# Optimization experiments

Hardware: AMD Instinct MI355X
Metric: run time of the kernel (lower is better)

The kernel has to match this reference:

```python
import jax, jax.numpy as jnp
import numpy as np

THETA_LO = 0.001
THETA_HI = 2.0
N_SUBSTEPS = 1
B, K, U, P, H, L = 256, 512, 16, 64, 256, 64
TH = 2 * P  # theta_dim: [decay rates | drives]


def setup_inputs() -> dict:
    key = jax.random.key(0)
    ks = jax.random.split(key, 12)
    s = 0.05
    return {
        "y0": jax.random.uniform(ks[0], (B, P), jnp.float32),
        "u_seq": jax.random.normal(ks[1], (B, K, U), jnp.float32),
        "dt_seq": jax.random.uniform(ks[2], (B, K), jnp.float32, 0.01, 0.1),
        "W_lift": jax.random.normal(ks[3], (L, U + P), jnp.float32) * s,
        "b_lift": jnp.zeros((L,), jnp.float32),
        "W_ih": jax.random.normal(ks[4], (3 * H, L), jnp.float32) * s,
        "b_ih": jnp.zeros((3 * H,), jnp.float32),
        "W_hh": jax.random.normal(ks[5], (3 * H, H), jnp.float32) * s,
        "b_hh": jnp.zeros((3 * H,), jnp.float32),
        "W_head": jax.random.normal(ks[6], (TH, H), jnp.float32) * s,
        "b_head": jnp.zeros((TH,), jnp.float32),
        "jump": jax.random.normal(ks[7], (U, P), jnp.float32) * s,
    }


def reference(y0, u_seq, dt_seq, W_lift, b_lift, W_ih, b_ih, W_hh, b_hh,
              W_head, b_head, jump):
    Pd = y0.shape[-1]

    def rhs(y, theta):
        # linear production/decay scaffold: y' = drive - decay * y
        return theta[:, Pd:] - theta[:, :Pd] * y

    def gru_cell(x, h):
        gi = x @ W_ih.T + b_ih            # [B, 3H]
        gh = h @ W_hh.T + b_hh            # [B, 3H]
        ir, iz, inn = jnp.split(gi, 3, axis=-1)
        hr, hz, hn = jnp.split(gh, 3, axis=-1)
        r = jax.nn.sigmoid(ir + hr)
        z = jax.nn.sigmoid(iz + hz)
        n = jnp.tanh(inn + r * hn)
        return (1.0 - z) * n + z * h

    def step(carry, inp):
        y_prev, h = carry
        u_k, dt_k = inp                   # [B,U], [B]
        y_in = jax.lax.stop_gradient(y_prev)  # .detach() in original
        feat = jnp.concatenate([u_k, y_in], axis=-1)
        x = jax.nn.silu(feat @ W_lift.T + b_lift)
        h = gru_cell(x, h)
        raw = h @ W_head.T + b_head
        theta = THETA_LO + (THETA_HI - THETA_LO) * jax.nn.sigmoid(raw)
        y = y_prev + u_k @ jump           # jump update
        hdt = (dt_k / N_SUBSTEPS)[:, None]
        for _ in range(N_SUBSTEPS):       # RK4 substeps
            k1 = rhs(y, theta)
            k2 = rhs(y + 0.5 * hdt * k1, theta)
            k3 = rhs(y + 0.5 * hdt * k2, theta)
            k4 = rhs(y + hdt * k3, theta)
            y = y + hdt / 6.0 * (k1 + 2.0 * k2 + 2.0 * k3 + k4)
        y = jnp.maximum(y, 0.0)           # clamp_min(0)
        return (y, h), (y, theta)

    Bd = y0.shape[0]
    Hd = W_hh.shape[1]
    h0 = jnp.zeros((Bd, Hd), y0.dtype)
    u_t = jnp.swapaxes(u_seq, 0, 1)       # [K,B,U]
    dt_t = dt_seq.T                       # [K,B]
    _, (y_out, th_out) = jax.lax.scan(step, (y0, h0), (u_t, dt_t))
    return jnp.swapaxes(y_out, 0, 1), jnp.swapaxes(th_out, 0, 1)
```

## Files before the change

kernel.cpp:

```cpp
#include <hip/hip_runtime.h>
#include <hip/hip_bf16.h>

#define BB 256
#define KK 512
#define UU 16
#define PP 64
#define HH 256
#define LL 64
#define THD 128
#define MB 16
#define NS 8
#define NG 16
#define NBLK (NG*NS)
#define NT 256

#define WHH_F 0
#define WIH_F 48
#define WHD_F 60
#define WLF_F 124
#define NFRG 136

#define FP2 104
#define XP2 72
#define TP2 132

#define HX_BUF 65536
#define HX_GRP 4096

typedef _Float16 f16;
typedef _Float16 f16x8 __attribute__((ext_vector_type(8)));
typedef float f32x4 __attribute__((ext_vector_type(4)));
typedef unsigned u32x4 __attribute__((ext_vector_type(4)));

__device__ __forceinline__ float sigm(float x) { return 1.f / (1.f + __expf(-x)); }
__device__ __forceinline__ f32x4 MFMA(f16x8 a, f16x8 b, f32x4 c) {
  return __builtin_amdgcn_mfma_f32_16x16x32_f16(a, b, c, 0, 0, 0);
}

#define GLD16_S(dst, p) \
  asm volatile("global_load_dwordx4 %0, %1, off sc0 sc1" : "=&v"(dst) : "v"(p))
#define GSTH_S(p, v) \
  asm volatile("global_store_short %0, %1, off sc0 sc1" :: "v"(p), "v"(v) : "memory")
#define VM0() do { asm volatile("s_waitcnt vmcnt(0)" ::: "memory"); \
                   __builtin_amdgcn_sched_barrier(0); } while (0)

struct SM {
  alignas(16) f16 frg[NFRG * 512];
  alignas(16) f16 x_M[MB * XP2];
  alignas(16) f16 f_M[MB * FP2];
  alignas(16) float th[MB * TP2];
  alignas(16) float ubuf[2][MB][UU];
  alignas(16) float jmp[UU * PP];
  float dts[2][MB];
  float bihs[96], bhhs[96];
  float bhead[THD];
  float blift[LL];
};

__device__ __forceinline__ void put_frag(f16* frg, int base_f, int ntK, int nt,
                                         int n16, int k, float v) {
  int kk = k >> 5, lgp = (k >> 3) & 3, j = k & 7;
  int lane = lgp * 16 + n16;
  frg[(base_f + nt * ntK + kk) * 512 + lane * 8 + j] = (f16)v;
}

#define FRG(FID) (*(const f16x8*)&sm.frg[(FID) * 512 + lane * 8])

__global__ __launch_bounds__(NT) void odernn_coop(
    const float* __restrict__ y0, const float* __restrict__ u_seq,
    const float* __restrict__ dt_seq, const float* __restrict__ W_lift,
    const float* __restrict__ b_lift, const float* __restrict__ W_ih,
    const float* __restrict__ b_ih, const float* __restrict__ W_hh,
    const float* __restrict__ b_hh, const float* __restrict__ W_head,
    const float* __restrict__ b_head, const float* __restrict__ jump,
    f16* __restrict__ hx,
    float* __restrict__ out_y, float* __restrict__ out_th) {
  __shared__ SM sm;
  const int t = threadIdx.x;
  const int lane = t & 63, wv = t >> 6, lm = lane & 15, lg = lane >> 4;
  const int bid = blockIdx.x, g = bid >> 3, ns = bid & 7;
  const int g16 = g * MB;
  const int ub = 32 * ns;

  for (int e = t; e < 96 * 256; e += NT) {
    int l = e >> 8, k = e & 255;
    int gate = l >> 5, ul = l & 31;
    put_frag(sm.frg, WHH_F, 8, l >> 4, l & 15, k, W_hh[(gate * 256 + ub + ul) * 256 + k]);
  }
  for (int e = t; e < 96 * 64; e += NT) {
    int l = e >> 6, k = e & 63;
    int gate = l >> 5, ul = l & 31;
    put_frag(sm.frg, WIH_F, 2, l >> 4, l & 15, k, W_ih[(gate * 256 + ub + ul) * 64 + k]);
  }
  for (int e = t; e < 128 * 256; e += NT) {
    int l = e >> 8, k = e & 255;
    put_frag(sm.frg, WHD_F, 8, l >> 4, l & 15, k, W_head[l * 256 + k]);
  }
  for (int e = t; e < 64 * 96; e += NT) {
    int l = e / 96, k = e - l * 96;
    float v = (k < UU + PP) ? W_lift[l * 80 + k] : 0.f;
    put_frag(sm.frg, WLF_F, 3, l >> 4, l & 15, k, v);
  }
  if (t < 96) { int gate = t >> 5, ul = t & 31;
    sm.bihs[t] = b_ih[gate * 256 + ub + ul];
    sm.bhhs[t] = b_hh[gate * 256 + ub + ul]; }
  if (t < THD) sm.bhead[t] = b_head[t];
  if (t < LL)  sm.blift[t] = b_lift[t];
  for (int e = t; e < UU * PP; e += NT) sm.jmp[e] = jump[e];
  for (int e = t; e < MB * FP2; e += NT) sm.f_M[e] = (f16)0.f;
  __syncthreads();
  if (t < 128) { int m = t >> 3, q = t & 7;
    float2 uv = *(const float2*)&u_seq[((size_t)(g16 + m) * KK) * UU + 2 * q];
    sm.ubuf[0][m][2 * q] = uv.x; sm.ubuf[0][m][2 * q + 1] = uv.y;
    sm.f_M[m * FP2 + 2 * q] = (f16)uv.x; sm.f_M[m * FP2 + 2 * q + 1] = (f16)uv.y; }
  if (t < MB) sm.dts[0][t] = dt_seq[(size_t)(g16 + t) * KK];
  const int rm = t >> 4, rp = (t & 15) * 4;
  float yr[4];
  { float4 yv = *(const float4*)&y0[(size_t)(g16 + rm) * PP + rp];
    yr[0] = yv.x; yr[1] = yv.y; yr[2] = yv.z; yr[3] = yv.w;
    sm.f_M[rm * FP2 + UU + rp]     = (f16)yv.x;
    sm.f_M[rm * FP2 + UU + rp + 1] = (f16)yv.y;
    sm.f_M[rm * FP2 + UU + rp + 2] = (f16)yv.z;
    sm.f_M[rm * FP2 + UU + rp + 3] = (f16)yv.w; }
  float ho[4] = {0.f, 0.f, 0.f, 0.f};
  f16x8 G0 = {}, G1 = {}, G2 = {}, G3 = {}, G4 = {}, G5 = {}, G6 = {}, G7 = {};
  __syncthreads();

#pragma unroll 1
  for (int j = 0; j < KK; ++j) {
    const int cb = j & 1, nb = cb ^ 1;
    const int negepoch = (j >> 1) & 1;
    f32x4 aR = {0.f,0.f,0.f,0.f}, aZ = aR, aI = aR, aH = aR;
    const int ntr = wv, ntz = 2 + wv, ntn = 4 + wv;

    if (wv < 2) {
#define GR(kk, Gk) \
      aR = MFMA(Gk, FRG(WHH_F + ntr * 8 + kk), aR); \
      aZ = MFMA(Gk, FRG(WHH_F + ntz * 8 + kk), aZ); \
      aH = MFMA(Gk, FRG(WHH_F + ntn * 8 + kk), aH);
      GR(0, G0) GR(1, G1) GR(2, G2) GR(3, G3)
      GR(4, G4) GR(5, G5) GR(6, G6) GR(7, G7)
#undef GR
    } else {
      const int t0 = 2 * (wv - 2), t1 = t0 + 1;
      const f16* fr = sm.f_M + lm * FP2 + lg * 8;
      f16x8 F0 = *(const f16x8*)(fr);
      f16x8 F1 = *(const f16x8*)(fr + 32);
      f16x8 F2 = *(const f16x8*)(fr + 64);
      f32x4 ax0 = {0.f, 0.f, 0.f, 0.f}, ax1 = ax0;
      ax0 = MFMA(F0, FRG(WLF_F + t0 * 3 + 0), ax0);
      ax1 = MFMA(F0, FRG(WLF_F + t1 * 3 + 0), ax1);
      ax0 = MFMA(F1, FRG(WLF_F + t0 * 3 + 1), ax0);
      ax1 = MFMA(F1, FRG(WLF_F + t1 * 3 + 1), ax1);
      ax0 = MFMA(F2, FRG(WLF_F + t0 * 3 + 2), ax0);
      ax1 = MFMA(F2, FRG(WLF_F + t1 * 3 + 2), ax1);
      const int c0 = t0 * 16 + lm, c1 = t1 * 16 + lm;
      const float bl0 = sm.blift[c0], bl1 = sm.blift[c1];
#pragma unroll
      for (int r = 0; r < 4; ++r) {
        float v0 = ax0[r] + bl0;
        sm.x_M[(4 * lg + r) * XP2 + c0] = (f16)(v0 * sigm(v0));
        float v1 = ax1[r] + bl1;
        sm.x_M[(4 * lg + r) * XP2 + c1] = (f16)(v1 * sigm(v1));
      }
    }
    __syncthreads();

    if (wv < 2) {
      const f16* xr = sm.x_M + lm * XP2 + lg * 8;
      f16x8 X0 = *(const f16x8*)(xr);
      f16x8 X1 = *(const f16x8*)(xr + 32);
      aR = MFMA(X0, FRG(WIH_F + ntr * 2 + 0), aR);
      aZ = MFMA(X0, FRG(WIH_F + ntz * 2 + 0), aZ);
      aI = MFMA(X0, FRG(WIH_F + ntn * 2 + 0), aI);
      aR = MFMA(X1, FRG(WIH_F + ntr * 2 + 1), aR);
      aZ = MFMA(X1, FRG(WIH_F + ntz * 2 + 1), aZ);
      aI = MFMA(X1, FRG(WIH_F + ntn * 2 + 1), aI);
      const int ul = 16 * wv + lm;
      const float br = sm.bihs[ul] + sm.bhhs[ul];
      const float bz = sm.bihs[32 + ul] + sm.bhhs[32 + ul];
      const float bi = sm.bihs[64 + ul];
      const float bh2 = sm.bhhs[64 + ul];
      const float sgn = negepoch ? -1.f : 1.f;
      f16* hw = hx + cb * HX_BUF + g * HX_GRP + ub + ul;
#pragma unroll
      for (int r = 0; r < 4; ++r) {
        float rr = sigm(aR[r] + br);
        float zz = sigm(aZ[r] + bz);
        float nn = 2.f * sigm(2.f * (aI[r] + bi + rr * (aH[r] + bh2))) - 1.f;
        float hv = (1.f - zz) * nn + zz * ho[r];
        ho[r] = hv;
        f16 h16 = (f16)(sgn * (hv + 2.f));
        unsigned hv32 = (unsigned)__builtin_bit_cast(unsigned short, h16);
        GSTH_S(hw + (4 * lg + r) * HH, hv32);
      }
    } else if (j + 1 < KK) {
      const int idx = t - 128;
      const int m = idx >> 3, q = idx & 7;
      float2 uv = *(const float2*)&u_seq[((size_t)(g16 + m) * KK + (j + 1)) * UU + 2 * q];
      sm.ubuf[nb][m][2 * q] = uv.x; sm.ubuf[nb][m][2 * q + 1] = uv.y;
      sm.f_M[m * FP2 + 2 * q] = (f16)uv.x; sm.f_M[m * FP2 + 2 * q + 1] = (f16)uv.y;
      if (idx < MB) sm.dts[nb][idx] = dt_seq[(size_t)(g16 + idx) * KK + (j + 1)];
    }

    {
      const unsigned want = negepoch ? 0x80008000u : 0u;
      const f16* hb2 = hx + cb * HX_BUF + g * HX_GRP + lm * HH + lg * 8;
      int guard = 4096; int ok;
      do {
        GLD16_S(G0, hb2);        GLD16_S(G1, hb2 + 32);
        GLD16_S(G2, hb2 + 64);   GLD16_S(G3, hb2 + 96);
        GLD16_S(G4, hb2 + 128);  GLD16_S(G5, hb2 + 160);
        GLD16_S(G6, hb2 + 192);  GLD16_S(G7, hb2 + 224);
        VM0();
        unsigned bad = 0u;
#define CK(Gk) { u32x4 u_ = __builtin_bit_cast(u32x4, Gk); \
        bad |= (u_.x ^ want) & 0x80008000u; bad |= (u_.y ^ want) & 0x80008000u; \
        bad |= (u_.z ^ want) & 0x80008000u; bad |= (u_.w ^ want) & 0x80008000u; }
        CK(G0) CK(G1) CK(G2) CK(G3) CK(G4) CK(G5) CK(G6) CK(G7)
#undef CK
        ok = __all(bad == 0u);
      } while (!ok && --guard);
      __builtin_amdgcn_sched_barrier(0);
      {
        const f16 m2 = (f16)(-2.f);
        const f16x8 M2 = {m2, m2, m2, m2, m2, m2, m2, m2};
        if (negepoch) {
          G0 = M2 - G0; G1 = M2 - G1; G2 = M2 - G2; G3 = M2 - G3;
          G4 = M2 - G4; G5 = M2 - G5; G6 = M2 - G6; G7 = M2 - G7;
        } else {
          G0 = G0 + M2; G1 = G1 + M2; G2 = G2 + M2; G3 = G3 + M2;
          G4 = G4 + M2; G5 = G5 + M2; G6 = G6 + M2; G7 = G7 + M2;
        }
      }
      f32x4 acc0 = {0.f,0.f,0.f,0.f}, acc1 = acc0;
#define HD(kk, Gk) \
      acc0 = MFMA(Gk, FRG(WHD_F + wv * 8 + kk), acc0); \
      acc1 = MFMA(Gk, FRG(WHD_F + (wv + 4) * 8 + kk), acc1);
      HD(0, G0) HD(1, G1) HD(2, G2) HD(3, G3)
      HD(4, G4) HD(5, G5) HD(6, G6) HD(7, G7)
#undef HD
      const float b0 = sm.bhead[wv * 16 + lm];
      const float b1 = sm.bhead[(wv + 4) * 16 + lm];
#pragma unroll
      for (int r = 0; r < 4; ++r) {
        sm.th[(4 * lg + r) * TP2 + wv * 16 + lm] = 0.001f + 1.999f * sigm(acc0[r] + b0);
        sm.th[(4 * lg + r) * TP2 + (wv + 4) * 16 + lm] = 0.001f + 1.999f * sigm(acc1[r] + b1);
      }
    }
    __syncthreads();

    {
      const float hdt = sm.dts[cb][rm];
      float4 outv;
#pragma unroll
      for (int i = 0; i < 4; ++i) {
        const int p = rp + i;
        float a = sm.th[rm * TP2 + p], dr = sm.th[rm * TP2 + 64 + p];
        float yv = yr[i];
#pragma unroll
        for (int uu = 0; uu < UU; ++uu)
          yv = fmaf(sm.ubuf[cb][rm][uu], sm.jmp[uu * PP + p], yv);
        float k1 = dr - a * yv;
        float k2 = dr - a * fmaf(0.5f * hdt, k1, yv);
        float k3 = dr - a * fmaf(0.5f * hdt, k2, yv);
        float k4 = dr - a * fmaf(hdt, k3, yv);
        yv = yv + (hdt * (1.f / 6.f)) * (k1 + 2.f * k2 + 2.f * k3 + k4);
        yv = fmaxf(yv, 0.f);
        yr[i] = yv;
        (&outv.x)[i] = yv;
        sm.f_M[rm * FP2 + UU + p] = (f16)yv;
      }
      if (ns == 0) {
        *(float4*)&out_y[((size_t)(g16 + rm) * KK + j) * PP + rp] = outv;
        const int c0 = (t & 15) * 8;
        *(float4*)&out_th[((size_t)(g16 + rm) * KK + j) * THD + c0] =
            *(const float4*)&sm.th[rm * TP2 + c0];
        *(float4*)&out_th[((size_t)(g16 + rm) * KK + j) * THD + c0 + 4] =
            *(const float4*)&sm.th[rm * TP2 + c0 + 4];
      }
    }
    __syncthreads();
  }
}

extern "C" void kernel_launch(void* const* d_in, const int* in_sizes, int n_in,
                              void* d_out, int out_size, void* d_ws, size_t ws_size,
                              hipStream_t stream) {
  (void)in_sizes; (void)n_in; (void)out_size; (void)ws_size;
  const float* y0     = (const float*)d_in[0];
  const float* u_seq  = (const float*)d_in[1];
  const float* dt_seq = (const float*)d_in[2];
  const float* W_lift = (const float*)d_in[3];
  const float* b_lift = (const float*)d_in[4];
  const float* W_ih   = (const float*)d_in[5];
  const float* b_ih   = (const float*)d_in[6];
  const float* W_hh   = (const float*)d_in[7];
  const float* b_hh   = (const float*)d_in[8];
  const float* W_head = (const float*)d_in[9];
  const float* b_head = (const float*)d_in[10];
  const float* jump   = (const float*)d_in[11];
  float* outy = (float*)d_out;
  float* outt = outy + (size_t)BB * KK * PP;
  f16* hx = (f16*)d_ws;

  hipMemsetAsync(d_ws, 0xAA, (size_t)2 * HX_BUF * sizeof(f16), stream);
  void* args[] = {
    (void*)&y0, (void*)&u_seq, (void*)&dt_seq, (void*)&W_lift, (void*)&b_lift,
    (void*)&W_ih, (void*)&b_ih, (void*)&W_hh, (void*)&b_hh, (void*)&W_head,
    (void*)&b_head, (void*)&jump, (void*)&hx, (void*)&outy, (void*)&outt
  };
  hipLaunchCooperativeKernel((const void*)odernn_coop, dim3(NBLK), dim3(NT),
                             args, 0, stream);
}
```

Measured before the change: 2.790 ms.

## Compute RK4 update in head-MFMA registers and drop theta LDS staging barrier

Each thread now handles the same parameter column it produced in the head MFMA accumulators. The ODE/RK4 update runs directly on those register values instead of writing theta to shared memory, syncing, and reading it back with a different thread mapping. This removes one __syncthreads per timestep and the theta LDS buffer. In exchange, output stores become scalar, strided per-element writes instead of float4 rows. An s_sleep is also added before the spin-poll on the hidden-state exchange buffer, which may reduce memory contention but can add latency.

```diff
diff --git a/kernel.cpp b/kernel.cpp
--- a/kernel.cpp
+++ b/kernel.cpp
@@ -22,7 +22,6 @@
 
 #define FP2 104
 #define XP2 72
-#define TP2 132
 
 #define HX_BUF 65536
 #define HX_GRP 4096
@@ -48,7 +47,6 @@
   alignas(16) f16 frg[NFRG * 512];
   alignas(16) f16 x_M[MB * XP2];
   alignas(16) f16 f_M[MB * FP2];
-  alignas(16) float th[MB * TP2];
   alignas(16) float ubuf[2][MB][UU];
   alignas(16) float jmp[UU * PP];
   float dts[2][MB];
@@ -114,14 +112,15 @@
     sm.ubuf[0][m][2 * q] = uv.x; sm.ubuf[0][m][2 * q + 1] = uv.y;
     sm.f_M[m * FP2 + 2 * q] = (f16)uv.x; sm.f_M[m * FP2 + 2 * q + 1] = (f16)uv.y; }
   if (t < MB) sm.dts[0][t] = dt_seq[(size_t)(g16 + t) * KK];
-  const int rm = t >> 4, rp = (t & 15) * 4;
+  const int myp = wv * 16 + lm;
   float yr[4];
-  { float4 yv = *(const float4*)&y0[(size_t)(g16 + rm) * PP + rp];
-    yr[0] = yv.x; yr[1] = yv.y; yr[2] = yv.z; yr[3] = yv.w;
-    sm.f_M[rm * FP2 + UU + rp]     = (f16)yv.x;
-    sm.f_M[rm * FP2 + UU + rp + 1] = (f16)yv.y;
-    sm.f_M[rm * FP2 + UU + rp + 2] = (f16)yv.z;
-    sm.f_M[rm * FP2 + UU + rp + 3] = (f16)yv.w; }
+#pragma unroll
+  for (int r = 0; r < 4; ++r) {
+    int m = 4 * lg + r;
+    float yv = y0[(size_t)(g16 + m) * PP + myp];
+    yr[r] = yv;
+    sm.f_M[m * FP2 + UU + myp] = (f16)yv;
+  }
   float ho[4] = {0.f, 0.f, 0.f, 0.f};
   f16x8 G0 = {}, G1 = {}, G2 = {}, G3 = {}, G4 = {}, G5 = {}, G6 = {}, G7 = {};
   __syncthreads();
@@ -204,6 +203,7 @@
     }
 
     {
+      asm volatile("s_sleep 8");
       const unsigned want = negepoch ? 0x80008000u : 0u;
       const f16* hb2 = hx + cb * HX_BUF + g * HX_GRP + lm * HH + lg * 8;
       int guard = 4096; int ok;
@@ -240,44 +240,38 @@
       HD(0, G0) HD(1, G1) HD(2, G2) HD(3, G3)
       HD(4, G4) HD(5, G5) HD(6, G6) HD(7, G7)
 #undef HD
-      const float b0 = sm.bhead[wv * 16 + lm];
-      const float b1 = sm.bhead[(wv + 4) * 16 + lm];
+      const float b0 = sm.bhead[myp];
+      const float b1 = sm.bhead[64 + myp];
+      float th0[4], th1[4];
 #pragma unroll
       for (int r = 0; r < 4; ++r) {
-        sm.th[(4 * lg + r) * TP2 + wv * 16 + lm] = 0.001f + 1.999f * sigm(acc0[r] + b0);
-        sm.th[(4 * lg + r) * TP2 + (wv + 4) * 16 + lm] = 0.001f + 1.999f * sigm(acc1[r] + b1);
-      }
-    }
-    __syncthreads();
-
-    {
-      const float hdt = sm.dts[cb][rm];
-      float4 outv;
-#pragma unroll
-      for (int i = 0; i < 4; ++i) {
-        const int p = rp + i;
-        float a = sm.th[rm * TP2 + p], dr = sm.th[rm * TP2 + 64 + p];
-        float yv = yr[i];
-#pragma unroll
-        for (int uu = 0; uu < UU; ++uu)
-          yv = fmaf(sm.ubuf[cb][rm][uu], sm.jmp[uu * PP + p], yv);
+        th0[r] = 0.001f + 1.999f * sigm(acc0[r] + b0);
+        th1[r] = 0.001f + 1.999f * sigm(acc1[r] + b1);
+      }
+      float jv[UU];
+#pragma unroll
+      for (int uu = 0; uu < UU; ++uu) jv[uu] = sm.jmp[uu * PP + myp];
+#pragma unroll
+      for (int r = 0; r < 4; ++r) {
+        const int m = 4 * lg + r;
+        const float hdt = sm.dts[cb][m];
+        float yv = yr[r];
+#pragma unroll
+        for (int uu = 0; uu < UU; ++uu) yv = fmaf(sm.ubuf[cb][m][uu], jv[uu], yv);
+        float a = th0[r], dr = th1[r];
         float k1 = dr - a * yv;
         float k2 = dr - a * fmaf(0.5f * hdt, k1, yv);
         float k3 = dr - a * fmaf(0.5f * hdt, k2, yv);
         float k4 = dr - a * fmaf(hdt, k3, yv);
         yv = yv + (hdt * (1.f / 6.f)) * (k1 + 2.f * k2 + 2.f * k3 + k4);
         yv = fmaxf(yv, 0.f);
-        yr[i] = yv;
-        (&outv.x)[i] = yv;
-        sm.f_M[rm * FP2 + UU + p] = (f16)yv;
-      }
-      if (ns == 0) {
-        *(float4*)&out_y[((size_t)(g16 + rm) * KK + j) * PP + rp] = outv;
-        const int c0 = (t & 15) * 8;
-        *(float4*)&out_th[((size_t)(g16 + rm) * KK + j) * THD + c0] =
-            *(const float4*)&sm.th[rm * TP2 + c0];
-        *(float4*)&out_th[((size_t)(g16 + rm) * KK + j) * THD + c0 + 4] =
-            *(const float4*)&sm.th[rm * TP2 + c0 + 4];
+        yr[r] = yv;
+        sm.f_M[m * FP2 + UU + myp] = (f16)yv;
+        if (ns == 0) {
+          out_y[((size_t)(g16 + m) * KK + j) * PP + myp] = yv;
+          out_th[((size_t)(g16 + m) * KK + j) * THD + myp] = a;
+          out_th[((size_t)(g16 + m) * KK + j) * THD + 64 + myp] = dr;
+        }
       }
     }
     __syncthreads();
```

Measured after the change: 2.830 ms. No clear change (+1.5%).
